# Kernel tuning notes

Hardware: AMD Instinct MI355X
Metric: run time of the kernel (lower is better)

## Reference

```python
import jax, jax.numpy as jnp
import numpy as np

D = 64
H = 4
HD = D // H
N_MOL, E_MOL = 2048, 32768
N_PROT, E_PROT = 8192, 262144
LN_EPS = 1e-5


def _lin_params(key, d_in, d_out):
    k1, k2 = jax.random.split(key)
    lim = 1.0 / np.sqrt(d_in)
    w = jax.random.uniform(k1, (d_in, d_out), minval=-lim, maxval=lim, dtype=jnp.float32)
    b = jax.random.uniform(k2, (d_out,), minval=-lim, maxval=lim, dtype=jnp.float32)
    return w, b


def setup_inputs() -> dict:
    key = jax.random.key(0)
    ks = jax.random.split(key, 20)
    inp = {
        'x_mol': jax.random.normal(ks[0], (N_MOL, D), dtype=jnp.float32),
        'edge_index_mol': jax.random.randint(ks[1], (2, E_MOL), 0, N_MOL),
        'edge_attr_mol': jax.random.normal(ks[2], (E_MOL, D), dtype=jnp.float32),
        'x_prot': jax.random.normal(ks[3], (N_PROT, D), dtype=jnp.float32),
        'edge_index_prot': jax.random.randint(ks[4], (2, E_PROT), 0, N_PROT),
        'edge_attr_prot': jax.random.normal(ks[5], (E_PROT, D), dtype=jnp.float32),
    }
    # GINE MLPs: Linear -> ReLU -> Linear
    inp['mol_w1'], inp['mol_b1'] = _lin_params(ks[6], D, D)
    inp['mol_w2'], inp['mol_b2'] = _lin_params(ks[7], D, D)
    inp['prot_w1'], inp['prot_b1'] = _lin_params(ks[8], D, D)
    inp['prot_w2'], inp['prot_b2'] = _lin_params(ks[9], D, D)
    # cross-attn mol->prot (query=mol, key/value=prot)
    inp['mp_wq'], inp['mp_bq'] = _lin_params(ks[10], D, D)
    inp['mp_wk'], inp['mp_bk'] = _lin_params(ks[11], D, D)
    inp['mp_wv'], inp['mp_bv'] = _lin_params(ks[12], D, D)
    # cross-attn prot->mol (query=prot, key/value=mol)
    inp['pm_wq'], inp['pm_bq'] = _lin_params(ks[13], D, D)
    inp['pm_wk'], inp['pm_bk'] = _lin_params(ks[14], D, D)
    inp['pm_wv'], inp['pm_bv'] = _lin_params(ks[15], D, D)
    # layer norms
    inp['ln_mol_g'] = jnp.ones((D,), jnp.float32)
    inp['ln_mol_b'] = jnp.zeros((D,), jnp.float32)
    inp['ln_prot_g'] = jnp.ones((D,), jnp.float32)
    inp['ln_prot_b'] = jnp.zeros((D,), jnp.float32)
    return inp


def _gine_conv(x, edge_index, edge_attr, w1, b1, w2, b2, n_nodes):
    # message: relu(x_j + edge_attr); aggregate: mean at target; update: MLP((1+eps)*x + aggr), eps=0
    src, dst = edge_index[0], edge_index[1]
    msg = jax.nn.relu(x[src] + edge_attr)                       # [E, D]
    ssum = jax.ops.segment_sum(msg, dst, num_segments=n_nodes)  # [N, D]
    cnt = jax.ops.segment_sum(jnp.ones((msg.shape[0],), msg.dtype), dst, num_segments=n_nodes)
    aggr = ssum / jnp.maximum(cnt, 1.0)[:, None]
    h = x + aggr
    h = jax.nn.relu(h @ w1 + b1) @ w2 + b2
    return h


def _cross_attn(q_nodes, k_nodes, wq, bq, wk, bk, wv, bv):
    Nq, Nk = q_nodes.shape[0], k_nodes.shape[0]
    Q = (q_nodes @ wq + bq).reshape(Nq, H, HD)
    K = (k_nodes @ wk + bk).reshape(Nk, H, HD)
    V = (k_nodes @ wv + bv).reshape(Nk, H, HD)
    scores = jnp.einsum('qhd,khd->hqk', Q, K) / np.sqrt(HD).astype(np.float32)
    attn = jax.nn.softmax(scores, axis=-1)                      # [H, Nq, Nk]
    out = jnp.einsum('hqk,khd->qhd', attn, V).reshape(Nq, D)
    return out


def _layer_norm(x, g, b):
    mu = jnp.mean(x, axis=-1, keepdims=True)
    var = jnp.mean(jnp.square(x - mu), axis=-1, keepdims=True)
    return (x - mu) * jax.lax.rsqrt(var + LN_EPS) * g + b


def reference(x_mol, edge_index_mol, edge_attr_mol, x_prot, edge_index_prot, edge_attr_prot,
              mol_w1, mol_b1, mol_w2, mol_b2, prot_w1, prot_b1, prot_w2, prot_b2,
              mp_wq, mp_bq, mp_wk, mp_bk, mp_wv, mp_bv,
              pm_wq, pm_bq, pm_wk, pm_bk, pm_wv, pm_bv,
              ln_mol_g, ln_mol_b, ln_prot_g, ln_prot_b):
    h_mol = jax.nn.relu(_gine_conv(x_mol, edge_index_mol, edge_attr_mol,
                                   mol_w1, mol_b1, mol_w2, mol_b2, x_mol.shape[0]))
    h_prot = jax.nn.relu(_gine_conv(x_prot, edge_index_prot, edge_attr_prot,
                                    prot_w1, prot_b1, prot_w2, prot_b2, x_prot.shape[0]))
    h_mol_attn = _cross_attn(h_mol, h_prot, mp_wq, mp_bq, mp_wk, mp_bk, mp_wv, mp_bv)
    h_prot_attn = _cross_attn(h_prot, h_mol, pm_wq, pm_bq, pm_wk, pm_bk, pm_wv, pm_bv)
    out_mol = _layer_norm(h_mol + h_mol_attn, ln_mol_g, ln_mol_b)
    out_prot = _layer_norm(h_prot + h_prot_attn, ln_prot_g, ln_prot_b)
    return out_mol, out_prot
```

## Files before the change

kernel.cpp:

```cpp
#include <hip/hip_runtime.h>

#define NM 2048
#define EM 32768
#define NP 8192
#define EP 262144

typedef __attribute__((ext_vector_type(8))) short short8;
typedef __attribute__((ext_vector_type(4))) short short4v;
typedef __attribute__((ext_vector_type(4))) float f32x4;

__device__ __forceinline__ unsigned short f2bf(float f) {
    unsigned int u = __float_as_uint(f);
    u = (u + 0x7fff + ((u >> 16) & 1)) >> 16;
    return (unsigned short)u;
}

__global__ __launch_bounds__(256) void edge_aggr_kernel(
    const float* __restrict__ x, const int* __restrict__ ei, const float* __restrict__ ea,
    float* __restrict__ ssum, float* __restrict__ cnt, int E)
{
    int idx = blockIdx.x * 256 + threadIdx.x;
    int total = E * 64;
    if (idx >= total) return;
    int e = idx >> 6;
    int c = idx & 63;
    int s = ei[e];
    int d = ei[E + e];
    float m = x[s * 64 + c] + ea[idx];
    m = fmaxf(m, 0.0f);
    atomicAdd(&ssum[d * 64 + c], m);
    if (c == 0) atomicAdd(&cnt[d], 1.0f);
}

__global__ __launch_bounds__(256) void gine_mlp_kernel(
    const float* __restrict__ x, const float* __restrict__ ssum, const float* __restrict__ cnt,
    const float* __restrict__ w1, const float* __restrict__ b1,
    const float* __restrict__ w2, const float* __restrict__ b2,
    float* __restrict__ out)
{
    __shared__ float sW1[4096], sW2[4096], sb1[64], sb2[64];
    __shared__ float sh0[16][64], sh1[16][64];
    int t = threadIdx.x;
    for (int i = t; i < 4096; i += 256) { sW1[i] = w1[i]; sW2[i] = w2[i]; }
    if (t < 64) { sb1[t] = b1[t]; sb2[t] = b2[t]; }
    int row0 = blockIdx.x * 16;
    for (int i = t; i < 16 * 64; i += 256) {
        int r = i >> 6, c = i & 63;
        int row = row0 + r;
        float cn = fmaxf(cnt[row], 1.0f);
        sh0[r][c] = x[row * 64 + c] + ssum[row * 64 + c] / cn;
    }
    __syncthreads();
    int j = t & 63, rs = t >> 6;
    for (int r = rs; r < 16; r += 4) {
        float a = sb1[j];
        #pragma unroll
        for (int c = 0; c < 64; c++) a += sh0[r][c] * sW1[c * 64 + j];
        sh1[r][j] = fmaxf(a, 0.0f);
    }
    __syncthreads();
    for (int r = rs; r < 16; r += 4) {
        float a = sb2[j];
        #pragma unroll
        for (int c = 0; c < 64; c++) a += sh1[r][c] * sW2[c * 64 + j];
        out[(size_t)(row0 + r) * 64 + j] = fmaxf(a, 0.0f);
    }
}

__global__ __launch_bounds__(256) void qkv_bf16_kernel(
    const float* __restrict__ x,
    const float* __restrict__ wq, const float* __restrict__ bq,
    const float* __restrict__ wk, const float* __restrict__ bk,
    const float* __restrict__ wv, const float* __restrict__ bv,
    unsigned short* __restrict__ Q, unsigned short* __restrict__ K,
    unsigned short* __restrict__ Vt, int N)
{
    __shared__ float sWq[4096], sWk[4096], sWv[4096];
    __shared__ float sbq[64], sbk[64], sbv[64];
    __shared__ float sh0[16][64];
    int t = threadIdx.x;
    for (int i = t; i < 4096; i += 256) { sWq[i] = wq[i]; sWk[i] = wk[i]; sWv[i] = wv[i]; }
    if (t < 64) { sbq[t] = bq[t]; sbk[t] = bk[t]; sbv[t] = bv[t]; }
    int row0 = blockIdx.x * 16;
    for (int i = t; i < 16 * 64; i += 256) {
        int r = i >> 6, c = i & 63;
        sh0[r][c] = x[(size_t)(row0 + r) * 64 + c];
    }
    __syncthreads();
    int j = t & 63, rs = t >> 6;
    for (int r = rs; r < 16; r += 4) {
        float aq = sbq[j], ak = sbk[j], av = sbv[j];
        #pragma unroll
        for (int c = 0; c < 64; c++) {
            float h = sh0[r][c];
            aq += h * sWq[c * 64 + j];
            ak += h * sWk[c * 64 + j];
            av += h * sWv[c * 64 + j];
        }
        size_t o = (size_t)(row0 + r) * 64 + j;
        Q[o] = f2bf(aq * 0.25f);
        K[o] = f2bf(ak);
        Vt[(size_t)j * N + row0 + r] = f2bf(av);
    }
}

__global__ __launch_bounds__(256) void attn_partial_kernel(
    const unsigned short* __restrict__ Q, const unsigned short* __restrict__ K,
    const unsigned short* __restrict__ Vt, float* __restrict__ partial,
    int Nk, int ncbits)
{
    __shared__ unsigned short plds[4][16][40];
    int t = threadIdx.x;
    int wave = t >> 6;
    int lane = t & 63;
    int qrow = lane & 15;
    int quad = lane >> 4;
    int NC = 1 << ncbits;
    int task = blockIdx.x * 4 + wave;
    int chunk = task & (NC - 1);
    int tmp = task >> ncbits;
    int h = tmp & 3;
    int qt = tmp >> 2;

    short8 qf = {};
    if (quad < 2)
        qf = *(const short8*)(Q + ((size_t)(qt * 16 + qrow)) * 64 + h * 16 + quad * 8);

    float m = -3.0e38f, l = 0.0f;
    f32x4 acc = {0.f, 0.f, 0.f, 0.f};
    const f32x4 zero4 = {0.f, 0.f, 0.f, 0.f};
    int kbase = chunk * 1024;

    for (int it = 0; it < 32; ++it) {
        int key0 = kbase + it * 32;
        short8 kf0 = {}, kf1 = {};
        if (quad < 2) {
            kf0 = *(const short8*)(K + ((size_t)(key0 + qrow)) * 64 + h * 16 + quad * 8);
            kf1 = *(const short8*)(K + ((size_t)(key0 + 16 + qrow)) * 64 + h * 16 + quad * 8);
        }
        short8 vf = *(const short8*)(Vt + ((size_t)(h * 16 + qrow)) * Nk + key0 + quad * 8);

        f32x4 s0 = __builtin_amdgcn_mfma_f32_16x16x32_bf16(kf0, qf, zero4, 0, 0, 0);
        f32x4 s1 = __builtin_amdgcn_mfma_f32_16x16x32_bf16(kf1, qf, zero4, 0, 0, 0);

        float tmax = fmaxf(fmaxf(fmaxf(s0.x, s0.y), fmaxf(s0.z, s0.w)),
                           fmaxf(fmaxf(s1.x, s1.y), fmaxf(s1.z, s1.w)));
        tmax = fmaxf(tmax, __shfl_xor(tmax, 16, 64));
        tmax = fmaxf(tmax, __shfl_xor(tmax, 32, 64));
        float mnew = fmaxf(m, tmax);
        float alpha = __expf(m - mnew);
        float p00 = __expf(s0.x - mnew), p01 = __expf(s0.y - mnew);
        float p02 = __expf(s0.z - mnew), p03 = __expf(s0.w - mnew);
        float p10 = __expf(s1.x - mnew), p11 = __expf(s1.y - mnew);
        float p12 = __expf(s1.z - mnew), p13 = __expf(s1.w - mnew);
        l = l * alpha + (((p00 + p01) + (p02 + p03)) + ((p10 + p11) + (p12 + p13)));
        acc.x *= alpha; acc.y *= alpha; acc.z *= alpha; acc.w *= alpha;

        short4v pk0, pk1;
        pk0.x = (short)f2bf(p00); pk0.y = (short)f2bf(p01);
        pk0.z = (short)f2bf(p02); pk0.w = (short)f2bf(p03);
        pk1.x = (short)f2bf(p10); pk1.y = (short)f2bf(p11);
        pk1.z = (short)f2bf(p12); pk1.w = (short)f2bf(p13);
        *(short4v*)&plds[wave][qrow][quad * 4] = pk0;
        *(short4v*)&plds[wave][qrow][16 + quad * 4] = pk1;
        short8 pf = *(short8*)&plds[wave][qrow][quad * 8];

        acc = __builtin_amdgcn_mfma_f32_16x16x32_bf16(vf, pf, acc, 0, 0, 0);
        m = mnew;
    }

    float ltot = l + __shfl_xor(l, 16, 64);
    ltot += __shfl_xor(ltot, 32, 64);

    float* pb = partial + (size_t)task * 288;
    *(f32x4*)&pb[qrow * 16 + quad * 4] = acc;
    if (quad == 0) { pb[256 + qrow] = m; pb[272 + qrow] = ltot; }
}

__global__ __launch_bounds__(256) void merge_ln_kernel(
    const float* __restrict__ partial, const float* __restrict__ hbuf,
    const float* __restrict__ g, const float* __restrict__ bia,
    float* __restrict__ out, int NC)
{
    int row = blockIdx.x * 4 + (threadIdx.x >> 6);
    int c = threadIdx.x & 63;
    int hi = c >> 4, d = c & 15;
    int qt = row >> 4, ql = row & 15;
    const float* base = partial + (size_t)(qt * 4 + hi) * NC * 288;
    float M = -3.0e38f;
    for (int cc = 0; cc < NC; ++cc) M = fmaxf(M, base[cc * 288 + 256 + ql]);
    float L = 0.0f, A = 0.0f;
    for (int cc = 0; cc < NC; ++cc) {
        float w = __expf(base[cc * 288 + 256 + ql] - M);
        L += base[cc * 288 + 272 + ql] * w;
        A += base[cc * 288 + ql * 16 + d] * w;
    }
    float v = hbuf[(size_t)row * 64 + c] + A / L;
    float s = v;
    #pragma unroll
    for (int o = 32; o >= 1; o >>= 1) s += __shfl_xor(s, o, 64);
    float mu = s * (1.0f / 64.0f);
    float dv = v - mu;
    float sq = dv * dv;
    #pragma unroll
    for (int o = 32; o >= 1; o >>= 1) sq += __shfl_xor(sq, o, 64);
    float var = sq * (1.0f / 64.0f);
    out[(size_t)row * 64 + c] = dv * rsqrtf(var + 1e-5f) * g[c] + bia[c];
}

extern "C" void kernel_launch(void* const* d_in, const int* in_sizes, int n_in,
                              void* d_out, int out_size, void* d_ws, size_t ws_size,
                              hipStream_t stream)
{
    const float* x_mol   = (const float*)d_in[0];
    const int*   ei_mol  = (const int*)  d_in[1];
    const float* ea_mol  = (const float*)d_in[2];
    const float* x_prot  = (const float*)d_in[3];
    const int*   ei_prot = (const int*)  d_in[4];
    const float* ea_prot = (const float*)d_in[5];
    const float* mol_w1  = (const float*)d_in[6];
    const float* mol_b1  = (const float*)d_in[7];
    const float* mol_w2  = (const float*)d_in[8];
    const float* mol_b2  = (const float*)d_in[9];
    const float* prot_w1 = (const float*)d_in[10];
    const float* prot_b1 = (const float*)d_in[11];
    const float* prot_w2 = (const float*)d_in[12];
    const float* prot_b2 = (const float*)d_in[13];
    const float* mp_wq = (const float*)d_in[14]; const float* mp_bq = (const float*)d_in[15];
    const float* mp_wk = (const float*)d_in[16]; const float* mp_bk = (const float*)d_in[17];
    const float* mp_wv = (const float*)d_in[18]; const float* mp_bv = (const float*)d_in[19];
    const float* pm_wq = (const float*)d_in[20]; const float* pm_bq = (const float*)d_in[21];
    const float* pm_wk = (const float*)d_in[22]; const float* pm_bk = (const float*)d_in[23];
    const float* pm_wv = (const float*)d_in[24]; const float* pm_bv = (const float*)d_in[25];
    const float* ln_mol_g  = (const float*)d_in[26];
    const float* ln_mol_b  = (const float*)d_in[27];
    const float* ln_prot_g = (const float*)d_in[28];
    const float* ln_prot_b = (const float*)d_in[29];

    float* ws = (float*)d_ws;
    float* ssum_mol  = ws;
    float* ssum_prot = ssum_mol + 131072;
    float* cnt_mol   = ssum_prot + 524288;
    float* cnt_prot  = cnt_mol + 2048;
    float* h_mol     = cnt_prot + 8192;
    float* h_prot    = h_mol + 131072;
    float* partial   = h_prot + 524288;
    unsigned short* bf = (unsigned short*)(partial + 1179648);
    unsigned short* Qm  = bf;
    unsigned short* Km  = Qm + 131072;
    unsigned short* Vtm = Km + 131072;
    unsigned short* Qp  = Vtm + 131072;
    unsigned short* Kp  = Qp + 524288;
    unsigned short* Vtp = Kp + 524288;

    hipMemsetAsync(ws, 0, (size_t)(131072 + 524288 + 2048 + 8192) * sizeof(float), stream);

    edge_aggr_kernel<<<EM * 64 / 256, 256, 0, stream>>>(x_mol, ei_mol, ea_mol, ssum_mol, cnt_mol, EM);
    edge_aggr_kernel<<<EP * 64 / 256, 256, 0, stream>>>(x_prot, ei_prot, ea_prot, ssum_prot, cnt_prot, EP);

    gine_mlp_kernel<<<NM / 16, 256, 0, stream>>>(x_mol, ssum_mol, cnt_mol, mol_w1, mol_b1, mol_w2, mol_b2, h_mol);
    gine_mlp_kernel<<<NP / 16, 256, 0, stream>>>(x_prot, ssum_prot, cnt_prot, prot_w1, prot_b1, prot_w2, prot_b2, h_prot);

    qkv_bf16_kernel<<<NM / 16, 256, 0, stream>>>(h_mol, mp_wq, mp_bq, pm_wk, pm_bk, pm_wv, pm_bv, Qm, Km, Vtm, NM);
    qkv_bf16_kernel<<<NP / 16, 256, 0, stream>>>(h_prot, pm_wq, pm_bq, mp_wk, mp_bk, mp_wv, mp_bv, Qp, Kp, Vtp, NP);

    float* out = (float*)d_out;

    attn_partial_kernel<<<1024, 256, 0, stream>>>(Qm, Kp, Vtp, partial, NP, 3);
    merge_ln_kernel<<<NM / 4, 256, 0, stream>>>(partial, h_mol, ln_mol_g, ln_mol_b, out, 8);

    attn_partial_kernel<<<1024, 256, 0, stream>>>(Qp, Km, Vtm, partial, NM, 1);
    merge_ln_kernel<<<NP / 4, 256, 0, stream>>>(partial, h_prot, ln_prot_g, ln_prot_b, out + 131072, 2);
}
```

Measured before the change: 348.8 us.

## Replace atomic edge scatter with CSR gather aggregation and fuse mol/prot launches

Builds a CSR by destination (histogram, scan, scatter) and replaces the per-element float atomicAdd scatter with a per-node wave gather that sums relu(x_src+edge_attr) without atomics. The mol and prot MLP and QKV launches are merged into single grids. The attention kernel now prefetches K/V one iteration ahead, folds log2e into Q so it can use exp2f, and packs P into 32-bit LDS stores. This removes heavy atomic contention on 16M float atomics, at the cost of extra small kernels, index arrays, and non-coalesced gathers of edge_attr through a permutation.

```diff
diff --git a/kernel.cpp b/kernel.cpp
--- a/kernel.cpp
+++ b/kernel.cpp
@@ -1,4 +1,5 @@
 #include <hip/hip_runtime.h>
+#include <hip/hip_bf16.h>
 
 #define NM 2048
 #define EM 32768
@@ -6,49 +7,151 @@
 #define EP 262144
 
 typedef __attribute__((ext_vector_type(8))) short short8;
-typedef __attribute__((ext_vector_type(4))) short short4v;
 typedef __attribute__((ext_vector_type(4))) float f32x4;
 
-__device__ __forceinline__ unsigned short f2bf(float f) {
-    unsigned int u = __float_as_uint(f);
-    u = (u + 0x7fff + ((u >> 16) & 1)) >> 16;
-    return (unsigned short)u;
-}
-
-__global__ __launch_bounds__(256) void edge_aggr_kernel(
-    const float* __restrict__ x, const int* __restrict__ ei, const float* __restrict__ ea,
-    float* __restrict__ ssum, float* __restrict__ cnt, int E)
+#define LOG2E 1.44269504088896340736f
+
+__device__ __forceinline__ unsigned short cvt_bf16(float f) {
+    __hip_bfloat16 h = __float2bfloat16(f);
+    return *(unsigned short*)&h;
+}
+__device__ __forceinline__ unsigned int pk_bf16(float a, float b) {
+    unsigned int lo = cvt_bf16(a), hi = cvt_bf16(b);
+    return lo | (hi << 16);
+}
+
+__global__ __launch_bounds__(256) void hist_kernel(
+    const int* __restrict__ ei_m, const int* __restrict__ ei_p,
+    int* __restrict__ cnt_m, int* __restrict__ cnt_p)
 {
     int idx = blockIdx.x * 256 + threadIdx.x;
-    int total = E * 64;
-    if (idx >= total) return;
-    int e = idx >> 6;
-    int c = idx & 63;
-    int s = ei[e];
-    int d = ei[E + e];
-    float m = x[s * 64 + c] + ea[idx];
-    m = fmaxf(m, 0.0f);
-    atomicAdd(&ssum[d * 64 + c], m);
-    if (c == 0) atomicAdd(&cnt[d], 1.0f);
+    if (idx < EM) atomicAdd(&cnt_m[ei_m[EM + idx]], 1);
+    int j = idx - EM;
+    if (j >= 0 && j < EP) atomicAdd(&cnt_p[ei_p[EP + j]], 1);
+}
+
+__global__ __launch_bounds__(256) void scan_kernel(
+    const int* __restrict__ cnt_m, const int* __restrict__ cnt_p,
+    int* __restrict__ start_m, int* __restrict__ start_p,
+    int* __restrict__ cur_m, int* __restrict__ cur_p)
+{
+    const int* cnt; int* start; int* cur; int n;
+    if (blockIdx.x == 0) { cnt = cnt_m; start = start_m; cur = cur_m; n = NM; }
+    else                 { cnt = cnt_p; start = start_p; cur = cur_p; n = NP; }
+    int per = n >> 8;
+    int tid = threadIdx.x;
+    int base = tid * per;
+    int s = 0;
+    for (int i = 0; i < per; i++) s += cnt[base + i];
+    __shared__ int wsum[4];
+    int lane = tid & 63, w = tid >> 6;
+    int v = s;
+    #pragma unroll
+    for (int off = 1; off < 64; off <<= 1) {
+        int u = __shfl_up(v, off, 64);
+        if (lane >= off) v += u;
+    }
+    if (lane == 63) wsum[w] = v;
+    __syncthreads();
+    int wo = 0;
+    for (int i = 0; i < w; i++) wo += wsum[i];
+    int run = wo + v - s;
+    for (int i = 0; i < per; i++) {
+        start[base + i] = run; cur[base + i] = run;
+        run += cnt[base + i];
+    }
+    if (tid == 255) start[n] = run;
+}
+
+__global__ __launch_bounds__(256) void scatter_kernel(
+    const int* __restrict__ ei_m, const int* __restrict__ ei_p,
+    int* __restrict__ cur_m, int* __restrict__ cur_p,
+    int* __restrict__ perm_m, int* __restrict__ perm_p,
+    int* __restrict__ srcs_m, int* __restrict__ srcs_p)
+{
+    int idx = blockIdx.x * 256 + threadIdx.x;
+    if (idx < EM) {
+        int d = ei_m[EM + idx];
+        int pos = atomicAdd(&cur_m[d], 1);
+        perm_m[pos] = idx; srcs_m[pos] = ei_m[idx];
+    }
+    int j = idx - EM;
+    if (j >= 0 && j < EP) {
+        int d = ei_p[EP + j];
+        int pos = atomicAdd(&cur_p[d], 1);
+        perm_p[pos] = j; srcs_p[pos] = ei_p[j];
+    }
+}
+
+__global__ __launch_bounds__(256) void node_aggr_kernel(
+    const float* __restrict__ x_m, const float* __restrict__ ea_m,
+    const int* __restrict__ start_m, const int* __restrict__ perm_m, const int* __restrict__ srcs_m,
+    const float* __restrict__ x_p, const float* __restrict__ ea_p,
+    const int* __restrict__ start_p, const int* __restrict__ perm_p, const int* __restrict__ srcs_p,
+    float* __restrict__ h0_m, float* __restrict__ h0_p)
+{
+    int wave = threadIdx.x >> 6, lane = threadIdx.x & 63;
+    int nid = blockIdx.x * 4 + wave;
+    const float *x, *ea; const int *start, *perm, *srcs; float* h0; int n;
+    if (nid < NM) { x = x_m; ea = ea_m; start = start_m; perm = perm_m; srcs = srcs_m; h0 = h0_m; n = nid; }
+    else          { x = x_p; ea = ea_p; start = start_p; perm = perm_p; srcs = srcs_p; h0 = h0_p; n = nid - NM; }
+    int b = start[n], e = start[n + 1];
+    int deg = e - b;
+    float acc = 0.f;
+    for (int c0 = 0; c0 < deg; c0 += 64) {
+        int rem = deg - c0;
+        int mcount = rem < 64 ? rem : 64;
+        int eL = 0, sL = 0;
+        if (lane < mcount) { eL = perm[b + c0 + lane]; sL = srcs[b + c0 + lane]; }
+        int j = 0;
+        for (; j + 3 < mcount; j += 4) {
+            int e0 = __shfl(eL, j, 64),   e1 = __shfl(eL, j + 1, 64);
+            int e2 = __shfl(eL, j + 2, 64), e3 = __shfl(eL, j + 3, 64);
+            int s0 = __shfl(sL, j, 64),   s1 = __shfl(sL, j + 1, 64);
+            int s2 = __shfl(sL, j + 2, 64), s3 = __shfl(sL, j + 3, 64);
+            float a0 = ea[(size_t)e0 * 64 + lane], a1 = ea[(size_t)e1 * 64 + lane];
+            float a2 = ea[(size_t)e2 * 64 + lane], a3 = ea[(size_t)e3 * 64 + lane];
+            float y0 = x[(size_t)s0 * 64 + lane], y1 = x[(size_t)s1 * 64 + lane];
+            float y2 = x[(size_t)s2 * 64 + lane], y3 = x[(size_t)s3 * 64 + lane];
+            acc += fmaxf(y0 + a0, 0.f);
+            acc += fmaxf(y1 + a1, 0.f);
+            acc += fmaxf(y2 + a2, 0.f);
+            acc += fmaxf(y3 + a3, 0.f);
+        }
+        for (; j < mcount; ++j) {
+            int e0 = __shfl(eL, j, 64);
+            int s0 = __shfl(sL, j, 64);
+            acc += fmaxf(x[(size_t)s0 * 64 + lane] + ea[(size_t)e0 * 64 + lane], 0.f);
+        }
+    }
+    float aggr = acc / fmaxf((float)deg, 1.f);
+    h0[(size_t)n * 64 + lane] = x[(size_t)n * 64 + lane] + aggr;
 }
 
 __global__ __launch_bounds__(256) void gine_mlp_kernel(
-    const float* __restrict__ x, const float* __restrict__ ssum, const float* __restrict__ cnt,
-    const float* __restrict__ w1, const float* __restrict__ b1,
-    const float* __restrict__ w2, const float* __restrict__ b2,
-    float* __restrict__ out)
-{
+    const float* __restrict__ h0_m, const float* __restrict__ h0_p,
+    const float* __restrict__ w1m, const float* __restrict__ b1m,
+    const float* __restrict__ w2m, const float* __restrict__ b2m,
+    const float* __restrict__ w1p, const float* __restrict__ b1p,
+    const float* __restrict__ w2p, const float* __restrict__ b2p,
+    float* __restrict__ hm, float* __restrict__ hp)
+{
+    const float *h0, *w1, *b1, *w2, *b2; float* out; int row0;
+    if (blockIdx.x < NM / 16) {
+        h0 = h0_m; w1 = w1m; b1 = b1m; w2 = w2m; b2 = b2m; out = hm;
+        row0 = blockIdx.x * 16;
+    } else {
+        h0 = h0_p; w1 = w1p; b1 = b1p; w2 = w2p; b2 = b2p; out = hp;
+        row0 = (blockIdx.x - NM / 16) * 16;
+    }
     __shared__ float sW1[4096], sW2[4096], sb1[64], sb2[64];
     __shared__ float sh0[16][64], sh1[16][64];
     int t = threadIdx.x;
     for (int i = t; i < 4096; i += 256) { sW1[i] = w1[i]; sW2[i] = w2[i]; }
     if (t < 64) { sb1[t] = b1[t]; sb2[t] = b2[t]; }
-    int row0 = blockIdx.x * 16;
     for (int i = t; i < 16 * 64; i += 256) {
         int r = i >> 6, c = i & 63;
-        int row = row0 + r;
-        float cn = fmaxf(cnt[row], 1.0f);
-        sh0[r][c] = x[row * 64 + c] + ssum[row * 64 + c] / cn;
+        sh0[r][c] = h0[(size_t)(row0 + r) * 64 + c];
     }
     __syncthreads();
     int j = t & 63, rs = t >> 6;
@@ -68,20 +171,31 @@
 }
 
 __global__ __launch_bounds__(256) void qkv_bf16_kernel(
-    const float* __restrict__ x,
-    const float* __restrict__ wq, const float* __restrict__ bq,
-    const float* __restrict__ wk, const float* __restrict__ bk,
-    const float* __restrict__ wv, const float* __restrict__ bv,
-    unsigned short* __restrict__ Q, unsigned short* __restrict__ K,
-    unsigned short* __restrict__ Vt, int N)
-{
+    const float* __restrict__ hm, const float* __restrict__ hp,
+    const float* __restrict__ wq_m, const float* __restrict__ bq_m,
+    const float* __restrict__ wk_m, const float* __restrict__ bk_m,
+    const float* __restrict__ wv_m, const float* __restrict__ bv_m,
+    const float* __restrict__ wq_p, const float* __restrict__ bq_p,
+    const float* __restrict__ wk_p, const float* __restrict__ bk_p,
+    const float* __restrict__ wv_p, const float* __restrict__ bv_p,
+    unsigned short* __restrict__ Qm, unsigned short* __restrict__ Km, unsigned short* __restrict__ Vtm,
+    unsigned short* __restrict__ Qp, unsigned short* __restrict__ Kp, unsigned short* __restrict__ Vtp)
+{
+    const float *x, *wq, *bq, *wk, *bk, *wv, *bv;
+    unsigned short *Q, *K, *Vt; int row0, N;
+    if (blockIdx.x < NM / 16) {
+        x = hm; wq = wq_m; bq = bq_m; wk = wk_m; bk = bk_m; wv = wv_m; bv = bv_m;
+        Q = Qm; K = Km; Vt = Vtm; N = NM; row0 = blockIdx.x * 16;
+    } else {
+        x = hp; wq = wq_p; bq = bq_p; wk = wk_p; bk = bk_p; wv = wv_p; bv = bv_p;
+        Q = Qp; K = Kp; Vt = Vtp; N = NP; row0 = (blockIdx.x - NM / 16) * 16;
+    }
     __shared__ float sWq[4096], sWk[4096], sWv[4096];
     __shared__ float sbq[64], sbk[64], sbv[64];
     __shared__ float sh0[16][64];
     int t = threadIdx.x;
     for (int i = t; i < 4096; i += 256) { sWq[i] = wq[i]; sWk[i] = wk[i]; sWv[i] = wv[i]; }
     if (t < 64) { sbq[t] = bq[t]; sbk[t] = bk[t]; sbv[t] = bv[t]; }
-    int row0 = blockIdx.x * 16;
     for (int i = t; i < 16 * 64; i += 256) {
         int r = i >> 6, c = i & 63;
         sh0[r][c] = x[(size_t)(row0 + r) * 64 + c];
@@ -98,9 +212,9 @@
             av += h * sWv[c * 64 + j];
         }
         size_t o = (size_t)(row0 + r) * 64 + j;
-        Q[o] = f2bf(aq * 0.25f);
-        K[o] = f2bf(ak);
-        Vt[(size_t)j * N + row0 + r] = f2bf(av);
+        Q[o] = cvt_bf16(aq * (0.25f * LOG2E));
+        K[o] = cvt_bf16(ak);
+        Vt[(size_t)j * N + row0 + r] = cvt_bf16(av);
     }
 }
 
@@ -109,7 +223,7 @@
     const unsigned short* __restrict__ Vt, float* __restrict__ partial,
     int Nk, int ncbits)
 {
-    __shared__ unsigned short plds[4][16][40];
+    __shared__ unsigned int plds[4][16][20];
     int t = threadIdx.x;
     int wave = t >> 6;
     int lane = t & 63;
@@ -130,15 +244,28 @@
     f32x4 acc = {0.f, 0.f, 0.f, 0.f};
     const f32x4 zero4 = {0.f, 0.f, 0.f, 0.f};
     int kbase = chunk * 1024;
+    const unsigned short* vrow = Vt + ((size_t)(h * 16 + qrow)) * Nk;
+
+    short8 kf0n = {}, kf1n = {}, vfn;
+    {
+        int key0 = kbase;
+        if (quad < 2) {
+            kf0n = *(const short8*)(K + ((size_t)(key0 + qrow)) * 64 + h * 16 + quad * 8);
+            kf1n = *(const short8*)(K + ((size_t)(key0 + 16 + qrow)) * 64 + h * 16 + quad * 8);
+        }
+        vfn = *(const short8*)(vrow + key0 + quad * 8);
+    }
 
     for (int it = 0; it < 32; ++it) {
-        int key0 = kbase + it * 32;
-        short8 kf0 = {}, kf1 = {};
-        if (quad < 2) {
-            kf0 = *(const short8*)(K + ((size_t)(key0 + qrow)) * 64 + h * 16 + quad * 8);
-            kf1 = *(const short8*)(K + ((size_t)(key0 + 16 + qrow)) * 64 + h * 16 + quad * 8);
+        short8 kf0 = kf0n, kf1 = kf1n, vf = vfn;
+        if (it < 31) {
+            int key0 = kbase + (it + 1) * 32;
+            if (quad < 2) {
+                kf0n = *(const short8*)(K + ((size_t)(key0 + qrow)) * 64 + h * 16 + quad * 8);
+                kf1n = *(const short8*)(K + ((size_t)(key0 + 16 + qrow)) * 64 + h * 16 + quad * 8);
+            }
+            vfn = *(const short8*)(vrow + key0 + quad * 8);
         }
-        short8 vf = *(const short8*)(Vt + ((size_t)(h * 16 + qrow)) * Nk + key0 + quad * 8);
 
         f32x4 s0 = __builtin_amdgcn_mfma_f32_16x16x32_bf16(kf0, qf, zero4, 0, 0, 0);
         f32x4 s1 = __builtin_amdgcn_mfma_f32_16x16x32_bf16(kf1, qf, zero4, 0, 0, 0);
@@ -148,22 +275,19 @@
         tmax = fmaxf(tmax, __shfl_xor(tmax, 16, 64));
         tmax = fmaxf(tmax, __shfl_xor(tmax, 32, 64));
         float mnew = fmaxf(m, tmax);
-        float alpha = __expf(m - mnew);
-        float p00 = __expf(s0.x - mnew), p01 = __expf(s0.y - mnew);
-        float p02 = __expf(s0.z - mnew), p03 = __expf(s0.w - mnew);
-        float p10 = __expf(s1.x - mnew), p11 = __expf(s1.y - mnew);
-        float p12 = __expf(s1.z - mnew), p13 = __expf(s1.w - mnew);
+        float alpha = exp2f(m - mnew);
+        float p00 = exp2f(s0.x - mnew), p01 = exp2f(s0.y - mnew);
+        float p02 = exp2f(s0.z - mnew), p03 = exp2f(s0.w - mnew);
+        float p10 = exp2f(s1.x - mnew), p11 = exp2f(s1.y - mnew);
+        float p12 = exp2f(s1.z - mnew), p13 = exp2f(s1.w - mnew);
         l = l * alpha + (((p00 + p01) + (p02 + p03)) + ((p10 + p11) + (p12 + p13)));
         acc.x *= alpha; acc.y *= alpha; acc.z *= alpha; acc.w *= alpha;
 
-        short4v pk0, pk1;
-        pk0.x = (short)f2bf(p00); pk0.y = (short)f2bf(p01);
-        pk0.z = (short)f2bf(p02); pk0.w = (short)f2bf(p03);
-        pk1.x = (short)f2bf(p10); pk1.y = (short)f2bf(p11);
-        pk1.z = (short)f2bf(p12); pk1.w = (short)f2bf(p13);
-        *(short4v*)&plds[wave][qrow][quad * 4] = pk0;
-        *(short4v*)&plds[wave][qrow][16 + quad * 4] = pk1;
-        short8 pf = *(short8*)&plds[wave][qrow][quad * 8];
+        plds[wave][qrow][quad * 2]     = pk_bf16(p00, p01);
+        plds[wave][qrow][quad * 2 + 1] = pk_bf16(p02, p03);
+        plds[wave][qrow][8 + quad * 2]     = pk_bf16(p10, p11);
+        plds[wave][qrow][8 + quad * 2 + 1] = pk_bf16(p12, p13);
+        short8 pf = *(short8*)&plds[wave][qrow][quad * 4];
 
         acc = __builtin_amdgcn_mfma_f32_16x16x32_bf16(vf, pf, acc, 0, 0, 0);
         m = mnew;
@@ -191,7 +315,7 @@
     for (int cc = 0; cc < NC; ++cc) M = fmaxf(M, base[cc * 288 + 256 + ql]);
     float L = 0.0f, A = 0.0f;
     for (int cc = 0; cc < NC; ++cc) {
-        float w = __expf(base[cc * 288 + 256 + ql] - M);
+        float w = exp2f(base[cc * 288 + 256 + ql] - M);
         L += base[cc * 288 + 272 + ql] * w;
         A += base[cc * 288 + ql * 16 + d] * w;
     }
@@ -238,14 +362,23 @@
     const float* ln_prot_b = (const float*)d_in[29];
 
     float* ws = (float*)d_ws;
-    float* ssum_mol  = ws;
-    float* ssum_prot = ssum_mol + 131072;
-    float* cnt_mol   = ssum_prot + 524288;
-    float* cnt_prot  = cnt_mol + 2048;
-    float* h_mol     = cnt_prot + 8192;
-    float* h_prot    = h_mol + 131072;
-    float* partial   = h_prot + 524288;
-    unsigned short* bf = (unsigned short*)(partial + 1179648);
+    float* h_mol   = ws;
+    float* h_prot  = h_mol + 131072;
+    float* partial = h_prot + 524288;
+    float* h0_mol  = partial;
+    float* h0_prot = h0_mol + 131072;
+    int* ip      = (int*)(partial + 1179648);
+    int* cnt_m   = ip;
+    int* cnt_p   = cnt_m + 2048;
+    int* start_m = cnt_p + 8192;
+    int* start_p = start_m + 2052;
+    int* cur_m   = start_p + 8196;
+    int* cur_p   = cur_m + 2048;
+    int* perm_m  = cur_p + 8192;
+    int* perm_p  = perm_m + 32768;
+    int* srcs_m  = perm_p + 262144;
+    int* srcs_p  = srcs_m + 32768;
+    unsigned short* bf = (unsigned short*)(srcs_p + 262144);
     unsigned short* Qm  = bf;
     unsigned short* Km  = Qm + 131072;
     unsigned short* Vtm = Km + 131072;
@@ -253,16 +386,25 @@
     unsigned short* Kp  = Qp + 524288;
     unsigned short* Vtp = Kp + 524288;
 
-    hipMemsetAsync(ws, 0, (size_t)(131072 + 524288 + 2048 + 8192) * sizeof(float), stream);
-
-    edge_aggr_kernel<<<EM * 64 / 256, 256, 0, stream>>>(x_mol, ei_mol, ea_mol, ssum_mol, cnt_mol, EM);
-    edge_aggr_kernel<<<EP * 64 / 256, 256, 0, stream>>>(x_prot, ei_prot, ea_prot, ssum_prot, cnt_prot, EP);
-
-    gine_mlp_kernel<<<NM / 16, 256, 0, stream>>>(x_mol, ssum_mol, cnt_mol, mol_w1, mol_b1, mol_w2, mol_b2, h_mol);
-    gine_mlp_kernel<<<NP / 16, 256, 0, stream>>>(x_prot, ssum_prot, cnt_prot, prot_w1, prot_b1, prot_w2, prot_b2, h_prot);
-
-    qkv_bf16_kernel<<<NM / 16, 256, 0, stream>>>(h_mol, mp_wq, mp_bq, pm_wk, pm_bk, pm_wv, pm_bv, Qm, Km, Vtm, NM);
-    qkv_bf16_kernel<<<NP / 16, 256, 0, stream>>>(h_prot, pm_wq, pm_bq, mp_wk, mp_bk, mp_wv, mp_bv, Qp, Kp, Vtp, NP);
+    hipMemsetAsync(cnt_m, 0, (size_t)(2048 + 8192) * sizeof(int), stream);
+
+    const int EB = (EM + EP) / 256;
+    hist_kernel<<<EB, 256, 0, stream>>>(ei_mol, ei_prot, cnt_m, cnt_p);
+    scan_kernel<<<2, 256, 0, stream>>>(cnt_m, cnt_p, start_m, start_p, cur_m, cur_p);
+    scatter_kernel<<<EB, 256, 0, stream>>>(ei_mol, ei_prot, cur_m, cur_p, perm_m, perm_p, srcs_m, srcs_p);
+    node_aggr_kernel<<<(NM + NP) / 4, 256, 0, stream>>>(
+        x_mol, ea_mol, start_m, perm_m, srcs_m,
+        x_prot, ea_prot, start_p, perm_p, srcs_p, h0_mol, h0_prot);
+
+    gine_mlp_kernel<<<(NM + NP) / 16, 256, 0, stream>>>(
+        h0_mol, h0_prot, mol_w1, mol_b1, mol_w2, mol_b2,
+        prot_w1, prot_b1, prot_w2, prot_b2, h_mol, h_prot);
+
+    qkv_bf16_kernel<<<(NM + NP) / 16, 256, 0, stream>>>(
+        h_mol, h_prot,
+        mp_wq, mp_bq, pm_wk, pm_bk, pm_wv, pm_bv,
+        pm_wq, pm_bq, mp_wk, mp_bk, mp_wv, mp_bv,
+        Qm, Km, Vtm, Qp, Kp, Vtp);
 
     float* out = (float*)d_out;
 
```

Measured after the change: 333.2 us. 1.05x faster.
